# Kernel tuning notes

Measured on AMD Instinct MI355X. Metric: run time of the kernel, lower is better.

The kernel has to match this reference:

```python
import jax, jax.numpy as jnp
import numpy as np

B, NG, FS, D, HH, C = 256, 32, 30, 1024, 3, 1024   # graphs, nodes/graph, feat, embed, heads, per-head dim
EPG = 160                                           # edges per graph
K1, K2, K3 = 26, 13, 4                              # ceil(0.8*32), ceil(0.5*26), ceil(0.3*13)


def gat_conv(x, src, dst, mask, W, a_src, a_dst, bias, N):
    """PyG GATConv (concat heads, negative_slope=0.2, add_self_loops=True), eval mode."""
    loop = jnp.arange(N, dtype=src.dtype)
    s = jnp.concatenate([src, loop])
    d = jnp.concatenate([dst, loop])
    m = jnp.concatenate([mask, jnp.ones((N,), bool)])
    xl = (x @ W).reshape(N, HH, C)                       # [N,H,C]
    al_s = jnp.sum(xl * a_src, -1)                       # [N,H]
    al_d = jnp.sum(xl * a_dst, -1)
    logits = jax.nn.leaky_relu(al_s[s] + al_d[d], negative_slope=0.2)  # [E,H]
    logits = jnp.where(m[:, None], logits, jnp.finfo(x.dtype).min)
    mx = jax.ops.segment_max(logits, d, num_segments=N)  # segment softmax over in-edges
    ex = jnp.where(m[:, None], jnp.exp(logits - mx[d]), 0.0)
    den = jax.ops.segment_sum(ex, d, num_segments=N)
    alpha = ex / den[d]
    out = jax.ops.segment_sum(alpha[:, :, None] * xl[s], d, num_segments=N)  # [N,H,C]
    return out.reshape(N, HH * C) + bias


def topk_pool(x, src, dst, mask, p, n_per, k):
    """PyG TopKPooling: score=tanh((x.p)/||p||); keep top-k per graph; gate kept x by score.
    Uniform graph size n_per -> static k. Dropped edges are masked, not removed."""
    score = jnp.tanh((x @ p) / jnp.linalg.norm(p))           # [B*n_per]
    _, idx = jax.lax.top_k(score.reshape(B, n_per), k)       # [B,k] local indices
    perm = (idx + (jnp.arange(B) * n_per)[:, None]).reshape(-1)
    x_new = x[perm] * score[perm][:, None]                   # [B*k, D]
    new_pos = jnp.full((B * n_per,), -1, jnp.int32).at[perm].set(
        jnp.arange(B * k, dtype=jnp.int32))
    ns, nd = new_pos[src], new_pos[dst]
    m = mask & (ns >= 0) & (nd >= 0)
    return x_new, jnp.where(m, ns, 0), jnp.where(m, nd, 0), m


def setup_inputs() -> dict:
    key = jax.random.key(0)
    ks = jax.random.split(key, 40)
    _n = lambda k, shape, s=0.05: jax.random.normal(k, shape, jnp.float32) * s

    x = jax.random.normal(ks[0], (B * NG, FS), jnp.float32)
    src_l = jax.random.randint(ks[1], (B, EPG), 0, NG)
    dst_l = jax.random.randint(ks[2], (B, EPG), 0, NG)
    offs = (jnp.arange(B) * NG)[:, None]
    edge_index = jnp.stack([(src_l + offs).reshape(-1),
                            (dst_l + offs).reshape(-1)]).astype(jnp.int32)
    batch_index = jnp.repeat(jnp.arange(B), NG).astype(jnp.int32)
    edge_attr = jax.random.normal(ks[3], (B * EPG, 6), jnp.float32)  # unused by model

    d = {"x": x, "edge_attr": edge_attr, "edge_index": edge_index, "batch_index": batch_index}
    ins = [FS, D, D]
    ki = 4
    for i, fin in enumerate(ins, 1):
        d[f"g{i}_W"] = _n(ks[ki], (fin, HH * C)); ki += 1
        d[f"g{i}_as"] = _n(ks[ki], (HH, C)); ki += 1
        d[f"g{i}_ad"] = _n(ks[ki], (HH, C)); ki += 1
        d[f"g{i}_b"] = jnp.zeros((HH * C,), jnp.float32)
        d[f"t{i}_W"] = _n(ks[ki], (HH * C, D)); ki += 1
        d[f"t{i}_b"] = jnp.zeros((D,), jnp.float32)
        d[f"p{i}"] = _n(ks[ki], (D,), 1.0); ki += 1
    d["l1_W"] = _n(ks[ki], (D, 1024)); ki += 1
    d["l1_b"] = jnp.zeros((1024,), jnp.float32)
    d["l2_W"] = _n(ks[ki], (1024, 1)); ki += 1
    d["l2_b"] = jnp.zeros((1,), jnp.float32)
    return d


def reference(x, edge_attr, edge_index, batch_index,
              g1_W, g1_as, g1_ad, g1_b, t1_W, t1_b, p1,
              g2_W, g2_as, g2_ad, g2_b, t2_W, t2_b, p2,
              g3_W, g3_as, g3_ad, g3_b, t3_W, t3_b, p3,
              l1_W, l1_b, l2_W, l2_b):
    src, dst = edge_index[0], edge_index[1]
    mask = jnp.ones(src.shape, bool)

    h = gat_conv(x, src, dst, mask, g1_W, g1_as, g1_ad, g1_b, B * NG)
    h = h @ t1_W + t1_b
    h, src, dst, mask = topk_pool(h, src, dst, mask, p1, NG, K1)
    x1 = h.reshape(B, K1, D).mean(1)                     # gap

    h = gat_conv(h, src, dst, mask, g2_W, g2_as, g2_ad, g2_b, B * K1)
    h = h @ t2_W + t2_b
    h, src, dst, mask = topk_pool(h, src, dst, mask, p2, K1, K2)
    x2 = h.reshape(B, K2, D).mean(1)

    h = gat_conv(h, src, dst, mask, g3_W, g3_as, g3_ad, g3_b, B * K2)
    h = h @ t3_W + t3_b
    h, src, dst, mask = topk_pool(h, src, dst, mask, p3, K2, K3)
    x3 = h.reshape(B, K3, D).mean(1)

    z = x1 + x2 + x3
    z = jax.nn.relu(z @ l1_W + l1_b)                     # dropout off (eval)
    return z @ l2_W + l2_b                               # [B, 1]
```

## Files before the change

### kernel.cpp

```cpp
#include <hip/hip_runtime.h>
#include <cstdint>
#include <cstddef>

#define EPG 160
#define HC  3072
#define DD  1024

typedef _Float16 f16x8 __attribute__((ext_vector_type(8)));
typedef _Float16 f16x2 __attribute__((ext_vector_type(2)));
typedef float    f32x4 __attribute__((ext_vector_type(4)));

__device__ __forceinline__ unsigned fenc(float f){
  unsigned u = __float_as_uint(f);
  return (u & 0x80000000u) ? ~u : (u | 0x80000000u);
}
__device__ __forceinline__ float fdec(unsigned u){
  return (u & 0x80000000u) ? __uint_as_float(u ^ 0x80000000u) : __uint_as_float(~u);
}

__device__ __forceinline__ void gload16(const void* g, void* l) {
  __builtin_amdgcn_global_load_lds((const __attribute__((address_space(1))) void*)g,
                                   (__attribute__((address_space(3))) void*)l, 16, 0, 0);
}

__global__ __launch_bounds__(256) void wtrans_kernel(
    const float* __restrict__ W, _Float16* __restrict__ WTh, _Float16* __restrict__ WTl,
    int K, int Nn)
{
  __shared__ float t[32][33];
  const int tx = threadIdx.x, ty = threadIdx.y;
  const int n0 = blockIdx.x * 32, k0 = blockIdx.y * 32;
  #pragma unroll
  for (int i = 0; i < 4; i++) {
    int k = k0 + ty + i * 8;
    t[ty + i * 8][tx] = (k < K) ? W[(size_t)k * Nn + n0 + tx] : 0.f;
  }
  __syncthreads();
  const int kt = k0 >> 5;
  const int c  = tx >> 3;
  const int w8 = tx & 7;
  #pragma unroll
  for (int i = 0; i < 4; i++) {
    int n = n0 + ty + i * 8;
    float v = t[tx][ty + i * 8];
    _Float16 h = (_Float16)v;
    float r = v - (float)h;
    int c2 = c ^ ((n >> 1) & 3);
    size_t addr = ((size_t)kt * Nn + n) * 32 + c2 * 8 + w8;
    WTh[addr] = h;
    WTl[addr] = (_Float16)r;
  }
}

__global__ __launch_bounds__(256) void prep_kernel(
    const float* __restrict__ p1, const float* __restrict__ p2, const float* __restrict__ p3,
    const float* __restrict__ g1W, const float* __restrict__ g1as, const float* __restrict__ g1ad,
    float* __restrict__ nrm, float* __restrict__ was, float* __restrict__ wad)
{
  const int b = blockIdx.x;
  const int tid = threadIdx.x;
  __shared__ float red[4];
  if (b < 3) {
    const float* p = b == 0 ? p1 : (b == 1 ? p2 : p3);
    float s = 0.f;
    for (int i = tid; i < DD; i += 256) { float v = p[i]; s += v * v; }
    #pragma unroll
    for (int off = 32; off; off >>= 1) s += __shfl_down(s, off);
    if ((tid & 63) == 0) red[tid >> 6] = s;
    __syncthreads();
    if (tid == 0) nrm[b] = sqrtf(red[0] + red[1] + red[2] + red[3]);
  } else {
    const int idx = b - 3;
    const int h = idx >> 1;
    const float* av = (idx & 1) ? g1ad : g1as;
    float* outv = (idx & 1) ? wad : was;
    for (int j = 0; j < 30; j++) {
      float s = 0.f;
      for (int c = tid; c < DD; c += 256)
        s += g1W[(size_t)j * HC + h * DD + c] * av[h * DD + c];
      #pragma unroll
      for (int off = 32; off; off >>= 1) s += __shfl_down(s, off);
      if ((tid & 63) == 0) red[tid >> 6] = s;
      __syncthreads();
      if (tid == 0) outv[h * 32 + j] = red[0] + red[1] + red[2] + red[3];
      __syncthreads();
    }
    if (tid == 0) { outv[h * 32 + 30] = 0.f; outv[h * 32 + 31] = 0.f; }
  }
}

__global__ __launch_bounds__(256) void gat_fused1(
    const float* __restrict__ x, const float* __restrict__ g1W,
    const float* __restrict__ was, const float* __restrict__ wad,
    const int* __restrict__ esrc, const int* __restrict__ edst,
    const float* __restrict__ gbias,
    _Float16* __restrict__ ATh, _Float16* __restrict__ ATl, int Mtot)
{
  const int g = blockIdx.x;
  const int h = blockIdx.y >> 1;
  const int half = blockIdx.y & 1;
  const int tid = threadIdx.x;
  const int base = g << 5;
  __shared__ float sx[32][32];
  __shared__ float sP[32][33];
  __shared__ float s_as[32], s_ad[32], s_mx[32], s_den[32];
  __shared__ unsigned s_mxu[32];

  for (int i = tid; i < 1024; i += 256) {
    int n = i >> 5, j = i & 31;
    sx[n][j] = (j < 30) ? x[(size_t)(base + n) * 30 + j] : 0.f;
  }
  for (int i = tid; i < 32 * 33; i += 256) ((float*)sP)[i] = 0.f;
  if (tid < 32) { s_mxu[tid] = 0u; s_den[tid] = 0.f; }
  __syncthreads();

  const int colb = h * DD + (half << 9);
  const int c = colb + (tid << 1);
  float w0[30], w1[30];
  #pragma unroll
  for (int j = 0; j < 30; j++) {
    float2 wv = *(const float2*)&g1W[(size_t)j * HC + c];
    w0[j] = wv.x; w1[j] = wv.y;
  }

  if (tid < 32) {
    float ps = 0.f, pd2 = 0.f;
    #pragma unroll
    for (int j = 0; j < 30; j++) {
      float xv = sx[tid][j];
      ps  += xv * was[h * 32 + j];
      pd2 += xv * wad[h * 32 + j];
    }
    s_as[tid] = ps; s_ad[tid] = pd2;
  }
  __syncthreads();

  int sl = 0, dl = 0;
  float lg = 0.f;
  if (tid < EPG) {
    int ei = g * EPG + tid;
    sl = esrc[ei] - base; dl = edst[ei] - base;
    float v = s_as[sl] + s_ad[dl];
    lg = v > 0.f ? v : 0.2f * v;
    atomicMax(&s_mxu[dl], fenc(lg));
  }
  float slg = 0.f;
  if (tid < 32) {
    float v = s_as[tid] + s_ad[tid];
    slg = v > 0.f ? v : 0.2f * v;
    atomicMax(&s_mxu[tid], fenc(slg));
  }
  __syncthreads();
  if (tid < 32) s_mx[tid] = fdec(s_mxu[tid]);
  __syncthreads();
  float ex = 0.f;
  if (tid < EPG) { ex = expf(lg - s_mx[dl]); atomicAdd(&s_den[dl], ex); }
  float exs = 0.f;
  if (tid < 32) { exs = expf(slg - s_mx[tid]); atomicAdd(&s_den[tid], exs); }
  __syncthreads();
  if (tid < EPG) atomicAdd(&sP[dl][sl], ex / s_den[dl]);
  if (tid < 32)  atomicAdd(&sP[tid][tid], exs / s_den[tid]);

  float xl0[32], xl1[32];
  #pragma unroll
  for (int n = 0; n < 32; n++) {
    float a0 = 0.f, a1 = 0.f;
    #pragma unroll
    for (int j = 0; j < 30; j++) {
      float xv = sx[n][j];
      a0 += xv * w0[j]; a1 += xv * w1[j];
    }
    xl0[n] = a0; xl1[n] = a1;
  }
  __syncthreads();

  const float b0 = gbias[c], b1 = gbias[c + 1];
  const int kt = c >> 5;
  const int ch = (c >> 3) & 3;
  const int j2 = c & 7;
  for (int n = 0; n < 32; n++) {
    float a0 = 0.f, a1 = 0.f;
    #pragma unroll
    for (int m = 0; m < 32; m++) {
      float p = sP[n][m];
      a0 += p * xl0[m]; a1 += p * xl1[m];
    }
    a0 += b0; a1 += b1;
    const int R = base + n;
    const int c2 = ch ^ ((R >> 1) & 3);
    const size_t ad = ((size_t)kt * Mtot + R) * 32 + c2 * 8 + j2;
    f16x2 hh, ll;
    _Float16 h0 = (_Float16)a0; hh[0] = h0; ll[0] = (_Float16)(a0 - (float)h0);
    _Float16 h1 = (_Float16)a1; hh[1] = h1; ll[1] = (_Float16)(a1 - (float)h1);
    *(f16x2*)&ATh[ad] = hh;
    *(f16x2*)&ATl[ad] = ll;
  }
}

__global__ __launch_bounds__(256) void mfma_gemm(
    const _Float16* __restrict__ ATh, const _Float16* __restrict__ ATl,
    const _Float16* __restrict__ BTh, const _Float16* __restrict__ BTl,
    const float* __restrict__ bias, float* __restrict__ C,
    int M, int N, int K,
    const float* __restrict__ avs, const float* __restrict__ avd,
    float* __restrict__ alsp, float* __restrict__ aldp,
    const float* __restrict__ pvec, float* __restrict__ scp)
{
  __shared__ __align__(16) char smem[2 * 32768];

  const int gx = N >> 7, gy = M >> 7;
  const int lid = blockIdx.x + gx * blockIdx.y;
  int vx, vy;
  const int G = gy & ~7;
  if (lid < gx * G) {
    const int sub = lid & 7, rest = lid >> 3;
    vx = rest % gx; vy = (rest / gx) * 8 + sub;
  } else {
    const int r = lid - gx * G;
    vx = r % gx; vy = G + r / gx;
  }
  const int brow = vy << 7, bcol = vx << 7;

  const int tid  = threadIdx.x;
  const int lane = tid & 63;
  const int w    = tid >> 6;
  const int wr   = (w >> 1) << 6, wc = (w & 1) << 6;
  const int wn   = w & 1;
  const int fr   = lane & 15, g4 = lane >> 4;

  f32x4 acc[4][4];
  #pragma unroll
  for (int m = 0; m < 4; m++)
    #pragma unroll
    for (int n = 0; n < 4; n++) acc[m][n] = (f32x4)0.0f;

  int aoff[4], boff[4];
  #pragma unroll
  for (int m = 0; m < 4; m++) {
    int r = wr + m * 16 + fr;
    aoff[m] = r * 64 + ((g4 ^ ((r >> 1) & 3)) << 4);
  }
  #pragma unroll
  for (int n = 0; n < 4; n++) {
    int r = wc + n * 16 + fr;
    boff[n] = r * 64 + ((g4 ^ ((r >> 1) & 3)) << 4);
  }

  const int ktiles = (K + 31) >> 5;

#define STAGE(ktv, buf)                                                    \
  do {                                                                     \
    char* bse = (buf);                                                     \
    const size_t ab = ((size_t)(ktv) * M + brow) << 6;                     \
    const size_t bb = ((size_t)(ktv) * N + bcol) << 6;                     \
    const char* gah = (const char*)ATh + ab + tid * 16;                    \
    const char* gal = (const char*)ATl + ab + tid * 16;                    \
    const char* gbh = (const char*)BTh + bb + tid * 16;                    \
    const char* gbl = (const char*)BTl + bb + tid * 16;                    \
    gload16(gah,        bse + tid * 16);                                   \
    gload16(gah + 4096, bse + tid * 16 + 4096);                            \
    gload16(gal,        bse + 8192 + tid * 16);                            \
    gload16(gal + 4096, bse + 8192 + tid * 16 + 4096);                     \
    gload16(gbh,        bse + 16384 + tid * 16);                           \
    gload16(gbh + 4096, bse + 16384 + tid * 16 + 4096);                    \
    gload16(gbl,        bse + 24576 + tid * 16);                           \
    gload16(gbl + 4096, bse + 24576 + tid * 16 + 4096);                    \
  } while (0)

  STAGE(0, smem);
  if (ktiles > 1) STAGE(1, smem + 32768);

  for (int kt = 0; kt < ktiles; kt++) {
    char* curb = smem + ((kt & 1) << 15);
    if (kt + 1 < ktiles) {
      asm volatile("s_waitcnt vmcnt(8)" ::: "memory");
    } else {
      asm volatile("s_waitcnt vmcnt(0)" ::: "memory");
    }
    __builtin_amdgcn_s_barrier();
    asm volatile("" ::: "memory");

    f16x8 ah[4], al[4], bh[4], bl[4];
    #pragma unroll
    for (int n = 0; n < 4; n++) {
      bh[n] = *(const f16x8*)(curb + 16384 + boff[n]);
      bl[n] = *(const f16x8*)(curb + 24576 + boff[n]);
    }
    #pragma unroll
    for (int m = 0; m < 4; m++) {
      ah[m] = *(const f16x8*)(curb + aoff[m]);
      al[m] = *(const f16x8*)(curb + 8192 + aoff[m]);
    }
    asm volatile("s_waitcnt lgkmcnt(0)" ::: "memory");
    __builtin_amdgcn_sched_barrier(0);
    __builtin_amdgcn_s_barrier();
    asm volatile("" ::: "memory");

    if (kt + 2 < ktiles) STAGE(kt + 2, curb);

    __builtin_amdgcn_s_setprio(1);
    #pragma unroll
    for (int m = 0; m < 4; m++) {
      #pragma unroll
      for (int n = 0; n < 4; n++) {
        acc[m][n] = __builtin_amdgcn_mfma_f32_16x16x32_f16(ah[m], bh[n], acc[m][n], 0, 0, 0);
        acc[m][n] = __builtin_amdgcn_mfma_f32_16x16x32_f16(al[m], bh[n], acc[m][n], 0, 0, 0);
        acc[m][n] = __builtin_amdgcn_mfma_f32_16x16x32_f16(ah[m], bl[n], acc[m][n], 0, 0, 0);
      }
    }
    __builtin_amdgcn_s_setprio(0);
    asm volatile("" ::: "memory");
  }
#undef STAGE

  const int crow0 = brow + wr + g4 * 4;
  const int ccol0 = bcol + wc + fr;
  #pragma unroll
  for (int n = 0; n < 4; n++) {
    const int col = ccol0 + n * 16;
    const float bv = bias ? bias[col] : 0.f;
    #pragma unroll
    for (int m = 0; m < 4; m++) {
      const int row = crow0 + m * 16;
      #pragma unroll
      for (int q = 0; q < 4; q++)
        C[(size_t)(row + q) * N + col] = acc[m][n][q] + bv;
    }
  }

  if (alsp) {
    const int h3 = bcol >> 10;
    const int slot = ((bcol & 1023) >> 6) + wn;
    #pragma unroll
    for (int m = 0; m < 4; m++) {
      #pragma unroll
      for (int q = 0; q < 4; q++) {
        float ps = 0.f, pd = 0.f;
        #pragma unroll
        for (int n = 0; n < 4; n++) {
          const int col = ccol0 + n * 16;
          const float v = acc[m][n][q];
          ps += v * avs[col]; pd += v * avd[col];
        }
        #pragma unroll
        for (int mk = 1; mk <= 8; mk <<= 1) {
          ps += __shfl_xor(ps, mk);
          pd += __shfl_xor(pd, mk);
        }
        if (fr == 0) {
          const int row = crow0 + m * 16 + q;
          alsp[row * 48 + h3 * 16 + slot] = ps;
          aldp[row * 48 + h3 * 16 + slot] = pd;
        }
      }
    }
  }
  if (scp) {
    const int slot = (bcol >> 6) + wn;
    #pragma unroll
    for (int m = 0; m < 4; m++) {
      #pragma unroll
      for (int q = 0; q < 4; q++) {
        float pp = 0.f;
        #pragma unroll
        for (int n = 0; n < 4; n++) {
          const int col = ccol0 + n * 16;
          pp += (acc[m][n][q] + bias[col]) * pvec[col];
        }
        #pragma unroll
        for (int mk = 1; mk <= 8; mk <<= 1) pp += __shfl_xor(pp, mk);
        if (fr == 0) scp[(crow0 + m * 16 + q) * 16 + slot] = pp;
      }
    }
  }
}

__global__ __launch_bounds__(256) void gat_agg(
    const float* __restrict__ xl, const float* __restrict__ alsp, const float* __restrict__ aldp,
    const int* __restrict__ esrc, const int* __restrict__ edst, const int* __restrict__ emask,
    const float* __restrict__ gbias, _Float16* __restrict__ ATh, _Float16* __restrict__ ATl,
    int npg, int Mtot)
{
  const int g = blockIdx.x;
  const int h = blockIdx.y >> 1;
  const int half = blockIdx.y & 1;
  const int tid = threadIdx.x;
  const int base = g * npg;
  __shared__ float sxl[32 * 512];
  __shared__ float s_as[32], s_ad[32], s_mx[32], s_den[32], s_self[32];
  __shared__ unsigned s_mxu[32];
  __shared__ float s_alpha[EPG];
  __shared__ int s_srcl[EPG];
  __shared__ int s_start[33];
  __shared__ int s_cnt[32], s_cur[32];
  __shared__ int s_list[EPG];

  const int colb = h * DD + (half << 9);
  for (int n = 0; n < npg; n++) {
    *(float2*)&sxl[(n << 9) + (tid << 1)] =
        *(const float2*)&xl[(size_t)(base + n) * HC + colb + (tid << 1)];
  }

  if (tid < npg) {
    const float* ps = alsp + (size_t)(base + tid) * 48 + h * 16;
    const float* pdp = aldp + (size_t)(base + tid) * 48 + h * 16;
    float ss = 0.f, dd2 = 0.f;
    #pragma unroll
    for (int s = 0; s < 16; s++) { ss += ps[s]; dd2 += pdp[s]; }
    s_as[tid] = ss;
    s_ad[tid] = dd2;
    s_mxu[tid] = 0u;
    s_den[tid] = 0.f;
    s_cnt[tid] = 0;
    s_cur[tid] = 0;
  }
  __syncthreads();

  int ok = 0, dl = 0;
  float lg = 0.f;
  if (tid < EPG) {
    int ei = g * EPG + tid;
    ok = emask ? emask[ei] : 1;
    if (ok) {
      int sl = esrc[ei] - base;
      dl = edst[ei] - base;
      s_srcl[tid] = sl;
      float v = s_as[sl] + s_ad[dl];
      lg = v > 0.f ? v : 0.2f * v;
      atomicMax(&s_mxu[dl], fenc(lg));
      atomicAdd(&s_cnt[dl], 1);
    }
  }
  float slg = 0.f;
  if (tid < npg) {
    float v = s_as[tid] + s_ad[tid];
    slg = v > 0.f ? v : 0.2f * v;
    atomicMax(&s_mxu[tid], fenc(slg));
  }
  __syncthreads();

  if (tid < npg) s_mx[tid] = fdec(s_mxu[tid]);
  if (tid == 0) {
    int run = 0;
    for (int n = 0; n < npg; n++) { s_start[n] = run; run += s_cnt[n]; }
    s_start[npg] = run;
  }
  __syncthreads();

  float ex = 0.f;
  if (tid < EPG && ok) {
    ex = expf(lg - s_mx[dl]);
    atomicAdd(&s_den[dl], ex);
    int p = s_start[dl] + atomicAdd(&s_cur[dl], 1);
    s_list[p] = tid;
  }
  if (tid < npg) {
    float e2 = expf(slg - s_mx[tid]);
    s_self[tid] = e2;
    atomicAdd(&s_den[tid], e2);
  }
  __syncthreads();

  if (tid < EPG && ok) s_alpha[tid] = ex / s_den[dl];
  if (tid < npg) s_self[tid] = s_self[tid] / s_den[tid];
  __syncthreads();

  const int c = colb + (tid << 1);
  const float b0 = gbias[c], b1 = gbias[c + 1];
  const int kt = c >> 5;
  const int ch = (c >> 3) & 3;
  const int j2 = c & 7;
  for (int n = 0; n < npg; n++) {
    const float2 v = *(const float2*)&sxl[(n << 9) + (tid << 1)];
    float a0 = s_self[n];
    float ax = a0 * v.x, ay = a0 * v.y;
    const int st = s_start[n], en = s_start[n + 1];
    for (int q = st; q < en; q++) {
      int e = s_list[q];
      float a = s_alpha[e];
      const float2 u = *(const float2*)&sxl[(s_srcl[e] << 9) + (tid << 1)];
      ax += a * u.x; ay += a * u.y;
    }
    ax += b0; ay += b1;
    const int R = base + n;
    const int c2 = ch ^ ((R >> 1) & 3);
    const size_t ad = ((size_t)kt * Mtot + R) * 32 + c2 * 8 + j2;
    f16x2 hh, ll;
    _Float16 h0 = (_Float16)ax; hh[0] = h0; ll[0] = (_Float16)(ax - (float)h0);
    _Float16 h1 = (_Float16)ay; hh[1] = h1; ll[1] = (_Float16)(ay - (float)h1);
    *(f16x2*)&ATh[ad] = hh;
    *(f16x2*)&ATl[ad] = ll;
  }
}

__global__ __launch_bounds__(256) void pool_kernel(
    const float* __restrict__ hbuf, const float* __restrict__ scp,
    const int* __restrict__ cs, const int* __restrict__ cd, const int* __restrict__ cm,
    int npg, int k, int Mnext,
    _Float16* __restrict__ ATh, _Float16* __restrict__ ATl,
    float* __restrict__ gap,
    int* __restrict__ ns, int* __restrict__ nd, int* __restrict__ nm,
    const float* __restrict__ nrm, int stage)
{
  int g = blockIdx.x, tid = threadIdx.x;
  __shared__ float ssc[32];
  __shared__ int sord[32];
  __shared__ int snp[32];
  __shared__ float sgp[2][1024];
  if (tid < npg) {
    const float* sp = scp + (size_t)(g * npg + tid) * 16;
    float s = 0.f;
    #pragma unroll
    for (int q = 0; q < 16; q++) s += sp[q];
    ssc[tid] = tanhf(s / nrm[stage]);
  }
  __syncthreads();
  if (tid == 0) {
    for (int i = 0; i < npg; i++) sord[i] = i;
    for (int i = 1; i < npg; i++) {
      int oi = sord[i]; float v = ssc[oi]; int j = i - 1;
      while (j >= 0 && ssc[sord[j]] < v) { sord[j + 1] = sord[j]; j--; }
      sord[j + 1] = oi;
    }
  }
  __syncthreads();
  if (tid < npg) snp[tid] = -1;
  __syncthreads();
  if (tid < k) snp[sord[tid]] = tid;
  __syncthreads();

  const int col0 = (tid & 127) << 3;
  const int rr = tid >> 7;
  const int kt = col0 >> 5;
  const int ch = (col0 >> 3) & 3;
  float part[8];
  #pragma unroll
  for (int j = 0; j < 8; j++) part[j] = 0.f;
  for (int r = rr; r < k; r += 2) {
    int ol = sord[r];
    float s = ssc[ol];
    const float* hr = hbuf + (size_t)(g * npg + ol) * DD + col0;
    float4 v0 = *(const float4*)hr;
    float4 v1 = *(const float4*)(hr + 4);
    float gv[8] = {v0.x * s, v0.y * s, v0.z * s, v0.w * s,
                   v1.x * s, v1.y * s, v1.z * s, v1.w * s};
    #pragma unroll
    for (int j = 0; j < 8; j++) part[j] += gv[j];
    if (ATh) {
      int R = g * k + r;
      int c2 = ch ^ ((R >> 1) & 3);
      size_t ad = ((size_t)kt * Mnext + R) * 32 + c2 * 8;
      f16x8 hh, ll;
      #pragma unroll
      for (int j = 0; j < 8; j++) {
        _Float16 hv = (_Float16)gv[j];
        hh[j] = hv; ll[j] = (_Float16)(gv[j] - (float)hv);
      }
      *(f16x8*)&ATh[ad] = hh;
      *(f16x8*)&ATl[ad] = ll;
    }
  }
  #pragma unroll
  for (int j = 0; j < 8; j++) sgp[rr][col0 + j] = part[j];
  __syncthreads();
  const float fk = (float)k;
  #pragma unroll
  for (int j = 0; j < 4; j++) {
    int cc = tid * 4 + j;
    gap[(size_t)g * DD + cc] = (sgp[0][cc] + sgp[1][cc]) / fk;
  }

  for (int e = tid; e < EPG; e += 256) {
    int ei = g * EPG + e;
    int ok = cm ? cm[ei] : 1;
    int m2 = 0, a = 0, b2 = 0;
    if (ok) {
      int sl = cs[ei] - g * npg, dl = cd[ei] - g * npg;
      int nsl = snp[sl], ndl = snp[dl];
      if (nsl >= 0 && ndl >= 0) { m2 = 1; a = g * k + nsl; b2 = g * k + ndl; }
    }
    ns[ei] = a; nd[ei] = b2; nm[ei] = m2;
  }
}

__global__ __launch_bounds__(256) void head_kernel(
    const float* __restrict__ X1, const float* __restrict__ X2, const float* __restrict__ X3,
    const float* __restrict__ l1W, const float* __restrict__ l1b,
    const float* __restrict__ l2W, float* __restrict__ partial)
{
  __shared__ float a[4][1024];
  __shared__ float red[4][4];
  const int tid = threadIdx.x;
  const int cg = blockIdx.x, rg = blockIdx.y;
  const int row0 = rg << 2;
  #pragma unroll
  for (int r = 0; r < 4; r++) {
    const size_t ro = (size_t)(row0 + r) << 10;
    #pragma unroll
    for (int jj = 0; jj < 4; jj++) {
      int j = tid + jj * 256;
      a[r][j] = X1[ro + j] + X2[ro + j] + X3[ro + j];
    }
  }
  __syncthreads();

  const int col = (cg << 8) + tid;
  float acc0 = 0.f, acc1 = 0.f, acc2 = 0.f, acc3 = 0.f;
  #pragma unroll 8
  for (int k = 0; k < 1024; k++) {
    float wv = l1W[((size_t)k << 10) + col];
    acc0 += a[0][k] * wv;
    acc1 += a[1][k] * wv;
    acc2 += a[2][k] * wv;
    acc3 += a[3][k] * wv;
  }
  const float bv = l1b[col], lw = l2W[col];
  float v0 = fmaxf(acc0 + bv, 0.f) * lw;
  float v1 = fmaxf(acc1 + bv, 0.f) * lw;
  float v2 = fmaxf(acc2 + bv, 0.f) * lw;
  float v3 = fmaxf(acc3 + bv, 0.f) * lw;
  #pragma unroll
  for (int off = 32; off; off >>= 1) {
    v0 += __shfl_down(v0, off);
    v1 += __shfl_down(v1, off);
    v2 += __shfl_down(v2, off);
    v3 += __shfl_down(v3, off);
  }
  const int lane = tid & 63, wid = tid >> 6;
  if (lane == 0) { red[wid][0] = v0; red[wid][1] = v1; red[wid][2] = v2; red[wid][3] = v3; }
  __syncthreads();
  if (tid < 4)
    partial[(size_t)(row0 + tid) * 4 + cg] =
        red[0][tid] + red[1][tid] + red[2][tid] + red[3][tid];
}

__global__ __launch_bounds__(256) void head2_kernel(
    const float* __restrict__ partial, const float* __restrict__ l2b,
    float* __restrict__ out)
{
  int r = threadIdx.x;
  out[r] = partial[r * 4 + 0] + partial[r * 4 + 1] +
           partial[r * 4 + 2] + partial[r * 4 + 3] + l2b[0];
}

extern "C" void kernel_launch(void* const* d_in, const int* in_sizes, int n_in,
                              void* d_out, int out_size, void* d_ws, size_t ws_size,
                              hipStream_t stream)
{
  (void)in_sizes; (void)n_in; (void)out_size; (void)ws_size;
  const float* x    = (const float*)d_in[0];
  const int*   eidx = (const int*)d_in[2];
  const float* g1W = (const float*)d_in[4];
  const float* g1as= (const float*)d_in[5];
  const float* g1ad= (const float*)d_in[6];
  const float* g1b = (const float*)d_in[7];
  const float* t1W = (const float*)d_in[8];
  const float* t1b = (const float*)d_in[9];
  const float* p1  = (const float*)d_in[10];
  const float* g2W = (const float*)d_in[11];
  const float* g2as= (const float*)d_in[12];
  const float* g2ad= (const float*)d_in[13];
  const float* g2b = (const float*)d_in[14];
  const float* t2W = (const float*)d_in[15];
  const float* t2b = (const float*)d_in[16];
  const float* p2  = (const float*)d_in[17];
  const float* g3W = (const float*)d_in[18];
  const float* g3as= (const float*)d_in[19];
  const float* g3ad= (const float*)d_in[20];
  const float* g3b = (const float*)d_in[21];
  const float* t3W = (const float*)d_in[22];
  const float* t3b = (const float*)d_in[23];
  const float* p3  = (const float*)d_in[24];
  const float* l1W = (const float*)d_in[25];
  const float* l1b = (const float*)d_in[26];
  const float* l2W = (const float*)d_in[27];
  const float* l2b = (const float*)d_in[28];
  float* outp = (float*)d_out;

  float* W = (float*)d_ws;
  size_t o = 0;
  float* bufA = W + o; o += (size_t)8192 * HC;
  float* bufB = W + o; o += (size_t)8192 * DD;
  _Float16* ATh = (_Float16*)(W + o); o += (size_t)96 * 8192 * 32 / 2;
  _Float16* ATl = (_Float16*)(W + o); o += (size_t)96 * 8192 * 32 / 2;
  float* ALSp = W + o; o += 8192 * 48;
  float* ALDp = W + o; o += 8192 * 48;
  float* SCp  = W + o; o += 8192 * 16;
  float* NRM = W + o; o += 4;
  float* WAS = W + o; o += 96;
  float* WAD = W + o; o += 96;
  float* X1  = W + o; o += 256 * DD;
  float* X2  = W + o; o += 256 * DD;
  float* X3  = W + o; o += 256 * DD;
  float* HP  = W + o; o += 256 * 4;
  int* E0s = (int*)(W + o); o += 40960;
  int* E0d = (int*)(W + o); o += 40960;
  int* E0m = (int*)(W + o); o += 40960;
  int* E1s = (int*)(W + o); o += 40960;
  int* E1d = (int*)(W + o); o += 40960;
  int* E1m = (int*)(W + o); o += 40960;
  _Float16* WTH = (_Float16*)(W + o); o += (3200 * 1024) / 2;
  _Float16* WTL = (_Float16*)(W + o); o += (3200 * 1024) / 2;

  const int* es1 = eidx;
  const int* ed1 = eidx + 40960;

  prep_kernel<<<9, 256, 0, stream>>>(p1, p2, p3, g1W, g1as, g1ad, NRM, WAS, WAD);
  gat_fused1<<<dim3(256, 6), 256, 0, stream>>>(x, g1W, WAS, WAD, es1, ed1, g1b,
                                               ATh, ATl, 8192);
  wtrans_kernel<<<dim3(32, 96), dim3(32, 8), 0, stream>>>(t1W, WTH, WTL, HC, DD);
  mfma_gemm<<<dim3(8, 64), 256, 0, stream>>>(ATh, ATl, WTH, WTL, t1b, bufB, 8192, DD, HC,
                                             nullptr, nullptr, nullptr, nullptr, p1, SCp);
  pool_kernel<<<256, 256, 0, stream>>>(bufB, SCp, es1, ed1, nullptr, 32, 26, 6656,
                                       ATh, ATl, X1, E0s, E0d, E0m, NRM, 0);

  wtrans_kernel<<<dim3(96, 32), dim3(32, 8), 0, stream>>>(g2W, WTH, WTL, DD, HC);
  mfma_gemm<<<dim3(24, 52), 256, 0, stream>>>(ATh, ATl, WTH, WTL, nullptr, bufA, 6656, HC, DD,
                                              g2as, g2ad, ALSp, ALDp, nullptr, nullptr);
  gat_agg<<<dim3(256, 6), 256, 0, stream>>>(bufA, ALSp, ALDp, E0s, E0d, E0m, g2b,
                                            ATh, ATl, 26, 6656);
  wtrans_kernel<<<dim3(32, 96), dim3(32, 8), 0, stream>>>(t2W, WTH, WTL, HC, DD);
  mfma_gemm<<<dim3(8, 52), 256, 0, stream>>>(ATh, ATl, WTH, WTL, t2b, bufB, 6656, DD, HC,
                                             nullptr, nullptr, nullptr, nullptr, p2, SCp);
  pool_kernel<<<256, 256, 0, stream>>>(bufB, SCp, E0s, E0d, E0m, 26, 13, 3328,
                                       ATh, ATl, X2, E1s, E1d, E1m, NRM, 1);

  wtrans_kernel<<<dim3(96, 32), dim3(32, 8), 0, stream>>>(g3W, WTH, WTL, DD, HC);
  mfma_gemm<<<dim3(24, 26), 256, 0, stream>>>(ATh, ATl, WTH, WTL, nullptr, bufA, 3328, HC, DD,
                                              g3as, g3ad, ALSp, ALDp, nullptr, nullptr);
  gat_agg<<<dim3(256, 6), 256, 0, stream>>>(bufA, ALSp, ALDp, E1s, E1d, E1m, g3b,
                                            ATh, ATl, 13, 3328);
  wtrans_kernel<<<dim3(32, 96), dim3(32, 8), 0, stream>>>(t3W, WTH, WTL, HC, DD);
  mfma_gemm<<<dim3(8, 26), 256, 0, stream>>>(ATh, ATl, WTH, WTL, t3b, bufB, 3328, DD, HC,
                                             nullptr, nullptr, nullptr, nullptr, p3, SCp);
  pool_kernel<<<256, 256, 0, stream>>>(bufB, SCp, E1s, E1d, E1m, 13, 4, 1024,
                                       nullptr, nullptr, X3, E0s, E0d, E0m, NRM, 2);

  head_kernel<<<dim3(4, 64), 256, 0, stream>>>(X1, X2, X3, l1W, l1b, l2W, HP);
  head2_kernel<<<1, 256, 0, stream>>>(HP, l2b, outp);
}
```

Before: 946.8 us.

## Compute TopK scores before transform GEMM and gather only kept rows

Scores are computed algebraically as (h·(W p) + b·p), using a precomputed projection V = W p fused into the GAT aggregation kernels. This lets top-k selection run before the 3072→1024 transform GEMM. The GEMM then gathers only the kept rows through a rowmap, applies the score gating, and writes the fp16 split operand for the next layer in its epilogue. This shrinks GEMM M (8192→6656, 6656→3328, 3328→1024) and removes the separate pool pass. The cost is a small vproj kernel, an extra gap kernel, and reassociated score arithmetic that could change top-k ordering on near ties.

Result: no change. 951.9 us (median of 2 runs) (+0.5%).

```diff
diff --git a/kernel.cpp b/kernel.cpp
--- a/kernel.cpp
+++ b/kernel.cpp
@@ -55,7 +55,9 @@
 __global__ __launch_bounds__(256) void prep_kernel(
     const float* __restrict__ p1, const float* __restrict__ p2, const float* __restrict__ p3,
     const float* __restrict__ g1W, const float* __restrict__ g1as, const float* __restrict__ g1ad,
-    float* __restrict__ nrm, float* __restrict__ was, float* __restrict__ wad)
+    const float* __restrict__ t1b, const float* __restrict__ t2b, const float* __restrict__ t3b,
+    float* __restrict__ nrm, float* __restrict__ was, float* __restrict__ wad,
+    float* __restrict__ bp)
 {
   const int b = blockIdx.x;
   const int tid = threadIdx.x;
@@ -69,7 +71,7 @@
     if ((tid & 63) == 0) red[tid >> 6] = s;
     __syncthreads();
     if (tid == 0) nrm[b] = sqrtf(red[0] + red[1] + red[2] + red[3]);
-  } else {
+  } else if (b < 9) {
     const int idx = b - 3;
     const int h = idx >> 1;
     const float* av = (idx & 1) ? g1ad : g1as;
@@ -86,7 +88,37 @@
       __syncthreads();
     }
     if (tid == 0) { outv[h * 32 + 30] = 0.f; outv[h * 32 + 31] = 0.f; }
-  }
+  } else {
+    const int i = b - 9;
+    const float* tb = i == 0 ? t1b : (i == 1 ? t2b : t3b);
+    const float* p = i == 0 ? p1 : (i == 1 ? p2 : p3);
+    float s = 0.f;
+    for (int c = tid; c < DD; c += 256) s += tb[c] * p[c];
+    #pragma unroll
+    for (int off = 32; off; off >>= 1) s += __shfl_down(s, off);
+    if ((tid & 63) == 0) red[tid >> 6] = s;
+    __syncthreads();
+    if (tid == 0) bp[i] = red[0] + red[1] + red[2] + red[3];
+  }
+}
+
+__global__ __launch_bounds__(64) void vproj_kernel(
+    const float* __restrict__ t1W, const float* __restrict__ t2W, const float* __restrict__ t3W,
+    const float* __restrict__ p1, const float* __restrict__ p2, const float* __restrict__ p3,
+    float* __restrict__ V)
+{
+  const int j = blockIdx.x;
+  const int i = blockIdx.y;
+  const float* Wm = i == 0 ? t1W : (i == 1 ? t2W : t3W);
+  const float* p  = i == 0 ? p1 : (i == 1 ? p2 : p3);
+  const int lane = threadIdx.x;
+  const float* row = Wm + (size_t)j * DD;
+  float s = 0.f;
+  #pragma unroll 4
+  for (int c = lane; c < DD; c += 64) s += row[c] * p[c];
+  #pragma unroll
+  for (int off = 32; off; off >>= 1) s += __shfl_down(s, off);
+  if (lane == 0) V[i * HC + j] = s;
 }
 
 __global__ __launch_bounds__(256) void gat_fused1(
@@ -94,7 +126,8 @@
     const float* __restrict__ was, const float* __restrict__ wad,
     const int* __restrict__ esrc, const int* __restrict__ edst,
     const float* __restrict__ gbias,
-    _Float16* __restrict__ ATh, _Float16* __restrict__ ATl, int Mtot)
+    _Float16* __restrict__ ATh, _Float16* __restrict__ ATl, int Mtot,
+    const float* __restrict__ V, float* __restrict__ scp)
 {
   const int g = blockIdx.x;
   const int h = blockIdx.y >> 1;
@@ -175,6 +208,8 @@
   __syncthreads();
 
   const float b0 = gbias[c], b1 = gbias[c + 1];
+  const float v0c = V[c], v1c = V[c + 1];
+  const int slot = blockIdx.y * 4 + (tid >> 6);
   const int kt = c >> 5;
   const int ch = (c >> 3) & 3;
   const int j2 = c & 7;
@@ -186,6 +221,10 @@
       a0 += p * xl0[m]; a1 += p * xl1[m];
     }
     a0 += b0; a1 += b1;
+    float sc = a0 * v0c + a1 * v1c;
+    #pragma unroll
+    for (int off = 32; off; off >>= 1) sc += __shfl_xor(sc, off);
+    if ((tid & 63) == 0) scp[(size_t)(base + n) * 24 + slot] = sc;
     const int R = base + n;
     const int c2 = ch ^ ((R >> 1) & 3);
     const size_t ad = ((size_t)kt * Mtot + R) * 32 + c2 * 8 + j2;
@@ -201,10 +240,11 @@
     const _Float16* __restrict__ ATh, const _Float16* __restrict__ ATl,
     const _Float16* __restrict__ BTh, const _Float16* __restrict__ BTl,
     const float* __restrict__ bias, float* __restrict__ C,
-    int M, int N, int K,
+    int M, int N, int K, int Msrc,
     const float* __restrict__ avs, const float* __restrict__ avd,
     float* __restrict__ alsp, float* __restrict__ aldp,
-    const float* __restrict__ pvec, float* __restrict__ scp)
+    const int* __restrict__ rowmap, const float* __restrict__ scores,
+    _Float16* __restrict__ AXh, _Float16* __restrict__ AXl)
 {
   __shared__ __align__(16) char smem[2 * 32768];
 
@@ -228,6 +268,18 @@
   const int wn   = w & 1;
   const int fr   = lane & 15, g4 = lane >> 4;
 
+  const int lr0 = tid >> 2;
+  int r0g, r1g;
+  if (rowmap) {
+    r0g = rowmap[brow + lr0];
+    r1g = rowmap[brow + 64 + lr0];
+  } else {
+    r0g = brow + lr0;
+    r1g = brow + 64 + lr0;
+  }
+  const int ch0 = (((tid & 3) ^ ((lr0 >> 1) & 3) ^ ((r0g >> 1) & 3)) << 4);
+  const int ch1 = (((tid & 3) ^ ((lr0 >> 1) & 3) ^ ((r1g >> 1) & 3)) << 4);
+
   f32x4 acc[4][4];
   #pragma unroll
   for (int m = 0; m < 4; m++)
@@ -248,23 +300,20 @@
 
   const int ktiles = (K + 31) >> 5;
 
-#define STAGE(ktv, buf)                                                    \
-  do {                                                                     \
-    char* bse = (buf);                                                     \
-    const size_t ab = ((size_t)(ktv) * M + brow) << 6;                     \
-    const size_t bb = ((size_t)(ktv) * N + bcol) << 6;                     \
-    const char* gah = (const char*)ATh + ab + tid * 16;                    \
-    const char* gal = (const char*)ATl + ab + tid * 16;                    \
-    const char* gbh = (const char*)BTh + bb + tid * 16;                    \
-    const char* gbl = (const char*)BTl + bb + tid * 16;                    \
-    gload16(gah,        bse + tid * 16);                                   \
-    gload16(gah + 4096, bse + tid * 16 + 4096);                            \
-    gload16(gal,        bse + 8192 + tid * 16);                            \
-    gload16(gal + 4096, bse + 8192 + tid * 16 + 4096);                     \
-    gload16(gbh,        bse + 16384 + tid * 16);                           \
-    gload16(gbh + 4096, bse + 16384 + tid * 16 + 4096);                    \
-    gload16(gbl,        bse + 24576 + tid * 16);                           \
-    gload16(gbl + 4096, bse + 24576 + tid * 16 + 4096);                    \
+#define STAGE(ktv, buf)                                                        \
+  do {                                                                         \
+    char* bse = (buf);                                                         \
+    const size_t a0ad = (((size_t)(ktv) * Msrc + r0g) << 6) + ch0;             \
+    const size_t a1ad = (((size_t)(ktv) * Msrc + r1g) << 6) + ch1;             \
+    const size_t bb = (((size_t)(ktv) * N + bcol) << 6) + tid * 16;            \
+    gload16((const char*)ATh + a0ad, bse + tid * 16);                          \
+    gload16((const char*)ATh + a1ad, bse + tid * 16 + 4096);                   \
+    gload16((const char*)ATl + a0ad, bse + 8192 + tid * 16);                   \
+    gload16((const char*)ATl + a1ad, bse + 8192 + tid * 16 + 4096);            \
+    gload16((const char*)BTh + bb,        bse + 16384 + tid * 16);             \
+    gload16((const char*)BTh + bb + 4096, bse + 16384 + tid * 16 + 4096);      \
+    gload16((const char*)BTl + bb,        bse + 24576 + tid * 16);             \
+    gload16((const char*)BTl + bb + 4096, bse + 24576 + tid * 16 + 4096);      \
   } while (0)
 
   STAGE(0, smem);
@@ -315,16 +364,41 @@
 
   const int crow0 = brow + wr + g4 * 4;
   const int ccol0 = bcol + wc + fr;
-  #pragma unroll
-  for (int n = 0; n < 4; n++) {
-    const int col = ccol0 + n * 16;
-    const float bv = bias ? bias[col] : 0.f;
+
+  if (scores) {
     #pragma unroll
     for (int m = 0; m < 4; m++) {
-      const int row = crow0 + m * 16;
       #pragma unroll
-      for (int q = 0; q < 4; q++)
-        C[(size_t)(row + q) * N + col] = acc[m][n][q] + bv;
+      for (int q = 0; q < 4; q++) {
+        const int row = crow0 + m * 16 + q;
+        const float s = scores[row];
+        #pragma unroll
+        for (int n = 0; n < 4; n++) {
+          const int col = ccol0 + n * 16;
+          const float gv = (acc[m][n][q] + bias[col]) * s;
+          C[(size_t)row * N + col] = gv;
+          if (AXh) {
+            const int c2 = ((col >> 3) & 3) ^ ((row >> 1) & 3);
+            const size_t ad = ((size_t)(col >> 5) * M + row) * 32 + c2 * 8 + (col & 7);
+            _Float16 hv = (_Float16)gv;
+            AXh[ad] = hv;
+            AXl[ad] = (_Float16)(gv - (float)hv);
+          }
+        }
+      }
+    }
+  } else {
+    #pragma unroll
+    for (int n = 0; n < 4; n++) {
+      const int col = ccol0 + n * 16;
+      const float bv = bias ? bias[col] : 0.f;
+      #pragma unroll
+      for (int m = 0; m < 4; m++) {
+        const int row = crow0 + m * 16;
+        #pragma unroll
+        for (int q = 0; q < 4; q++)
+          C[(size_t)(row + q) * N + col] = acc[m][n][q] + bv;
+      }
     }
   }
 
@@ -355,31 +429,13 @@
       }
     }
   }
-  if (scp) {
-    const int slot = (bcol >> 6) + wn;
-    #pragma unroll
-    for (int m = 0; m < 4; m++) {
-      #pragma unroll
-      for (int q = 0; q < 4; q++) {
-        float pp = 0.f;
-        #pragma unroll
-        for (int n = 0; n < 4; n++) {
-          const int col = ccol0 + n * 16;
-          pp += (acc[m][n][q] + bias[col]) * pvec[col];
-        }
-        #pragma unroll
-        for (int mk = 1; mk <= 8; mk <<= 1) pp += __shfl_xor(pp, mk);
-        if (fr == 0) scp[(crow0 + m * 16 + q) * 16 + slot] = pp;
-      }
-    }
-  }
 }
 
 __global__ __launch_bounds__(256) void gat_agg(
     const float* __restrict__ xl, const float* __restrict__ alsp, const float* __restrict__ aldp,
     const int* __restrict__ esrc, const int* __restrict__ edst, const int* __restrict__ emask,
     const float* __restrict__ gbias, _Float16* __restrict__ ATh, _Float16* __restrict__ ATl,
-    int npg, int Mtot)
+    int npg, int Mtot, const float* __restrict__ V, float* __restrict__ scp)
 {
   const int g = blockIdx.x;
   const int h = blockIdx.y >> 1;
@@ -467,6 +523,8 @@
 
   const int c = colb + (tid << 1);
   const float b0 = gbias[c], b1 = gbias[c + 1];
+  const float v0c = V[c], v1c = V[c + 1];
+  const int slot = blockIdx.y * 4 + (tid >> 6);
   const int kt = c >> 5;
   const int ch = (c >> 3) & 3;
   const int j2 = c & 7;
@@ -482,6 +540,10 @@
       ax += a * u.x; ay += a * u.y;
     }
     ax += b0; ay += b1;
+    float sc = ax * v0c + ay * v1c;
+    #pragma unroll
+    for (int off = 32; off; off >>= 1) sc += __shfl_xor(sc, off);
+    if ((tid & 63) == 0) scp[(size_t)(base + n) * 24 + slot] = sc;
     const int R = base + n;
     const int c2 = ch ^ ((R >> 1) & 3);
     const size_t ad = ((size_t)kt * Mtot + R) * 32 + c2 * 8 + j2;
@@ -493,26 +555,24 @@
   }
 }
 
-__global__ __launch_bounds__(256) void pool_kernel(
-    const float* __restrict__ hbuf, const float* __restrict__ scp,
+__global__ __launch_bounds__(256) void select_kernel(
+    const float* __restrict__ scp, const float* __restrict__ nrm,
+    const float* __restrict__ bp, int stage,
     const int* __restrict__ cs, const int* __restrict__ cd, const int* __restrict__ cm,
-    int npg, int k, int Mnext,
-    _Float16* __restrict__ ATh, _Float16* __restrict__ ATl,
-    float* __restrict__ gap,
-    int* __restrict__ ns, int* __restrict__ nd, int* __restrict__ nm,
-    const float* __restrict__ nrm, int stage)
+    int npg, int k,
+    int* __restrict__ rowmap, float* __restrict__ scores,
+    int* __restrict__ ns, int* __restrict__ nd, int* __restrict__ nm)
 {
   int g = blockIdx.x, tid = threadIdx.x;
   __shared__ float ssc[32];
   __shared__ int sord[32];
   __shared__ int snp[32];
-  __shared__ float sgp[2][1024];
   if (tid < npg) {
-    const float* sp = scp + (size_t)(g * npg + tid) * 16;
+    const float* sp = scp + (size_t)(g * npg + tid) * 24;
     float s = 0.f;
     #pragma unroll
-    for (int q = 0; q < 16; q++) s += sp[q];
-    ssc[tid] = tanhf(s / nrm[stage]);
+    for (int q = 0; q < 24; q++) s += sp[q];
+    ssc[tid] = tanhf((s + bp[stage]) / nrm[stage]);
   }
   __syncthreads();
   if (tid == 0) {
@@ -526,49 +586,12 @@
   __syncthreads();
   if (tid < npg) snp[tid] = -1;
   __syncthreads();
-  if (tid < k) snp[sord[tid]] = tid;
-  __syncthreads();
-
-  const int col0 = (tid & 127) << 3;
-  const int rr = tid >> 7;
-  const int kt = col0 >> 5;
-  const int ch = (col0 >> 3) & 3;
-  float part[8];
-  #pragma unroll
-  for (int j = 0; j < 8; j++) part[j] = 0.f;
-  for (int r = rr; r < k; r += 2) {
-    int ol = sord[r];
-    float s = ssc[ol];
-    const float* hr = hbuf + (size_t)(g * npg + ol) * DD + col0;
-    float4 v0 = *(const float4*)hr;
-    float4 v1 = *(const float4*)(hr + 4);
-    float gv[8] = {v0.x * s, v0.y * s, v0.z * s, v0.w * s,
-                   v1.x * s, v1.y * s, v1.z * s, v1.w * s};
-    #pragma unroll
-    for (int j = 0; j < 8; j++) part[j] += gv[j];
-    if (ATh) {
-      int R = g * k + r;
-      int c2 = ch ^ ((R >> 1) & 3);
-      size_t ad = ((size_t)kt * Mnext + R) * 32 + c2 * 8;
-      f16x8 hh, ll;
-      #pragma unroll
-      for (int j = 0; j < 8; j++) {
-        _Float16 hv = (_Float16)gv[j];
-        hh[j] = hv; ll[j] = (_Float16)(gv[j] - (float)hv);
-      }
-      *(f16x8*)&ATh[ad] = hh;
-      *(f16x8*)&ATl[ad] = ll;
-    }
-  }
-  #pragma unroll
-  for (int j = 0; j < 8; j++) sgp[rr][col0 + j] = part[j];
-  __syncthreads();
-  const float fk = (float)k;
-  #pragma unroll
-  for (int j = 0; j < 4; j++) {
-    int cc = tid * 4 + j;
-    gap[(size_t)g * DD + cc] = (sgp[0][cc] + sgp[1][cc]) / fk;
-  }
+  if (tid < k) {
+    snp[sord[tid]] = tid;
+    rowmap[g * k + tid] = g * npg + sord[tid];
+    scores[g * k + tid] = ssc[sord[tid]];
+  }
+  __syncthreads();
 
   for (int e = tid; e < EPG; e += 256) {
     int ei = g * EPG + e;
@@ -581,6 +604,20 @@
     }
     ns[ei] = a; nd[ei] = b2; nm[ei] = m2;
   }
+}
+
+__global__ __launch_bounds__(256) void gap_kernel(
+    const float* __restrict__ xb, int k, float* __restrict__ gap)
+{
+  const int g = blockIdx.x, tid = threadIdx.x;
+  float a0 = 0.f, a1 = 0.f, a2 = 0.f, a3 = 0.f;
+  for (int r = 0; r < k; r++) {
+    const float4 v = *(const float4*)&xb[(((size_t)(g * k + r)) << 10) + (tid << 2)];
+    a0 += v.x; a1 += v.y; a2 += v.z; a3 += v.w;
+  }
+  const float fk = (float)k;
+  float4 o = make_float4(a0 / fk, a1 / fk, a2 / fk, a3 / fk);
+  *(float4*)&gap[((size_t)g << 10) + (tid << 2)] = o;
 }
 
 __global__ __launch_bounds__(256) void head_kernel(
@@ -679,20 +716,27 @@
 
   float* W = (float*)d_ws;
   size_t o = 0;
-  float* bufA = W + o; o += (size_t)8192 * HC;
-  float* bufB = W + o; o += (size_t)8192 * DD;
-  _Float16* ATh = (_Float16*)(W + o); o += (size_t)96 * 8192 * 32 / 2;
-  _Float16* ATl = (_Float16*)(W + o); o += (size_t)96 * 8192 * 32 / 2;
+  float* bufA = W + o;
+  float* bufB = bufA;
+  o += (size_t)6656 * HC;
+  _Float16* ATAh = (_Float16*)(W + o); o += (size_t)96 * 8192 * 32 / 2;
+  _Float16* ATAl = (_Float16*)(W + o); o += (size_t)96 * 8192 * 32 / 2;
+  _Float16* AXh  = (_Float16*)(W + o); o += (size_t)32 * 6656 * 32 / 2;
+  _Float16* AXl  = (_Float16*)(W + o); o += (size_t)32 * 6656 * 32 / 2;
   float* ALSp = W + o; o += 8192 * 48;
   float* ALDp = W + o; o += 8192 * 48;
-  float* SCp  = W + o; o += 8192 * 16;
+  float* SCP  = W + o; o += 8192 * 24;
   float* NRM = W + o; o += 4;
+  float* BP  = W + o; o += 4;
   float* WAS = W + o; o += 96;
   float* WAD = W + o; o += 96;
+  float* V   = W + o; o += 3 * HC;
   float* X1  = W + o; o += 256 * DD;
   float* X2  = W + o; o += 256 * DD;
   float* X3  = W + o; o += 256 * DD;
   float* HP  = W + o; o += 256 * 4;
+  float* SSEL = W + o; o += 6656;
+  int* RMAP = (int*)(W + o); o += 6656;
   int* E0s = (int*)(W + o); o += 40960;
   int* E0d = (int*)(W + o); o += 40960;
   int* E0m = (int*)(W + o); o += 40960;
@@ -705,36 +749,52 @@
   const int* es1 = eidx;
   const int* ed1 = eidx + 40960;
 
-  prep_kernel<<<9, 256, 0, stream>>>(p1, p2, p3, g1W, g1as, g1ad, NRM, WAS, WAD);
+  prep_kernel<<<12, 256, 0, stream>>>(p1, p2, p3, g1W, g1as, g1ad, t1b, t2b, t3b,
+                                      NRM, WAS, WAD, BP);
+  vproj_kernel<<<dim3(HC, 3), 64, 0, stream>>>(t1W, t2W, t3W, p1, p2, p3, V);
+
   gat_fused1<<<dim3(256, 6), 256, 0, stream>>>(x, g1W, WAS, WAD, es1, ed1, g1b,
-                                               ATh, ATl, 8192);
+                                               ATAh, ATAl, 8192, V, SCP);
+  select_kernel<<<256, 256, 0, stream>>>(SCP, NRM, BP, 0, es1, ed1, nullptr, 32, 26,
+                                         RMAP, SSEL, E0s, E0d, E0m);
   wtrans_kernel<<<dim3(32, 96), dim3(32, 8), 0, stream>>>(t1W, WTH, WTL, HC, DD);
-  mfma_gemm<<<dim3(8, 64), 256, 0, stream>>>(ATh, ATl, WTH, WTL, t1b, bufB, 8192, DD, HC,
-                                             nullptr, nullptr, nullptr, nullptr, p1, SCp);
-  pool_kernel<<<256, 256, 0, stream>>>(bufB, SCp, es1, ed1, nullptr, 32, 26, 6656,
-                                       ATh, ATl, X1, E0s, E0d, E0m, NRM, 0);
+  mfma_gemm<<<dim3(8, 52), 256, 0, stream>>>(ATAh, ATAl, WTH, WTL, t1b, bufB,
+                                             6656, DD, HC, 8192,
+                                             nullptr, nullptr, nullptr, nullptr,
+                                             RMAP, SSEL, AXh, AXl);
+  gap_kernel<<<256, 256, 0, stream>>>(bufB, 26, X1);
 
   wtrans_kernel<<<dim3(96, 32), dim3(32, 8), 0, stream>>>(g2W, WTH, WTL, DD, HC);
-  mfma_gemm<<<dim3(24, 52), 256, 0, stream>>>(ATh, ATl, WTH, WTL, nullptr, bufA, 6656, HC, DD,
-                                              g2as, g2ad, ALSp, ALDp, nullptr, nullptr);
+  mfma_gemm<<<dim3(24, 52), 256, 0, stream>>>(AXh, AXl, WTH, WTL, nullptr, bufA,
+                                              6656, HC, DD, 6656,
+                                              g2as, g2ad, ALSp, ALDp,
+                                              nullptr, nullptr, nullptr, nullptr);
   gat_agg<<<dim3(256, 6), 256, 0, stream>>>(bufA, ALSp, ALDp, E0s, E0d, E0m, g2b,
-                                            ATh, ATl, 26, 6656);
+                                            ATAh, ATAl, 26, 6656, V + HC, SCP);
+  select_kernel<<<256, 256, 0, stream>>>(SCP, NRM, BP, 1, E0s, E0d, E0m, 26, 13,
+                                         RMAP, SSEL, E1s, E1d, E1m);
   wtrans_kernel<<<dim3(32, 96), dim3(32, 8), 0, stream>>>(t2W, WTH, WTL, HC, DD);
-  mfma_gemm<<<dim3(8, 52), 256, 0, stream>>>(ATh, ATl, WTH, WTL, t2b, bufB, 6656, DD, HC,
-                                             nullptr, nullptr, nullptr, nullptr, p2, SCp);
-  pool_kernel<<<256, 256, 0, stream>>>(bufB, SCp, E0s, E0d, E0m, 26, 13, 3328,
-                                       ATh, ATl, X2, E1s, E1d, E1m, NRM, 1);
+  mfma_gemm<<<dim3(8, 26), 256, 0, stream>>>(ATAh, ATAl, WTH, WTL, t2b, bufB,
+                                             3328, DD, HC, 6656,
+                                             nullptr, nullptr, nullptr, nullptr,
+                                             RMAP, SSEL, AXh, AXl);
+  gap_kernel<<<256, 256, 0, stream>>>(bufB, 13, X2);
 
   wtrans_kernel<<<dim3(96, 32), dim3(32, 8), 0, stream>>>(g3W, WTH, WTL, DD, HC);
-  mfma_gemm<<<dim3(24, 26), 256, 0, stream>>>(ATh, ATl, WTH, WTL, nullptr, bufA, 3328, HC, DD,
-                                              g3as, g3ad, ALSp, ALDp, nullptr, nullptr);
+  mfma_gemm<<<dim3(24, 26), 256, 0, stream>>>(AXh, AXl, WTH, WTL, nullptr, bufA,
+                                              3328, HC, DD, 3328,
+                                              g3as, g3ad, ALSp, ALDp,
+                                              nullptr, nullptr, nullptr, nullptr);
   gat_agg<<<dim3(256, 6), 256, 0, stream>>>(bufA, ALSp, ALDp, E1s, E1d, E1m, g3b,
-                                            ATh, ATl, 13, 3328);
+                                            ATAh, ATAl, 13, 3328, V + 2 * HC, SCP);
+  select_kernel<<<256, 256, 0, stream>>>(SCP, NRM, BP, 2, E1s, E1d, E1m, 13, 4,
+                                         RMAP, SSEL, E0s, E0d, E0m);
   wtrans_kernel<<<dim3(32, 96), dim3(32, 8), 0, stream>>>(t3W, WTH, WTL, HC, DD);
-  mfma_gemm<<<dim3(8, 26), 256, 0, stream>>>(ATh, ATl, WTH, WTL, t3b, bufB, 3328, DD, HC,
-                                             nullptr, nullptr, nullptr, nullptr, p3, SCp);
-  pool_kernel<<<256, 256, 0, stream>>>(bufB, SCp, E1s, E1d, E1m, 13, 4, 1024,
-                                       nullptr, nullptr, X3, E0s, E0d, E0m, NRM, 2);
+  mfma_gemm<<<dim3(8, 8), 256, 0, stream>>>(ATAh, ATAl, WTH, WTL, t3b, bufB,
+                                            1024, DD, HC, 3328,
+                                            nullptr, nullptr, nullptr, nullptr,
+                                            RMAP, SSEL, nullptr, nullptr);
+  gap_kernel<<<256, 256, 0, stream>>>(bufB, 4, X3);
 
   head_kernel<<<dim3(4, 64), 256, 0, stream>>>(X1, X2, X3, l1W, l1b, l2W, HP);
   head2_kernel<<<1, 256, 0, stream>>>(HP, l2b, outp);
```
